# Performance work log

Hardware: AMD Instinct MI355X
Metric: run time of the kernel (lower is better)

## Reference

```python
import jax, jax.numpy as jnp
import numpy as np

B, T, H, HW = 16, 32, 512, 32  # batch, timesteps, hidden channels, spatial size


def setup_inputs() -> dict:
    key = jax.random.key(0)
    k1, k2, k3, k4, k5 = jax.random.split(key, 5)
    x = jax.random.normal(k1, (B, T, HW, HW), dtype=jnp.float32)
    # cell conv: 1x1, (1 + H) -> 4H, with bias (k=1 default, padding 'same')
    W_conv = jax.random.normal(k2, (4 * H, 1 + H, 1, 1), dtype=jnp.float32) * 0.02
    b_conv = jax.random.normal(k3, (4 * H,), dtype=jnp.float32) * 0.02
    # post conv: 3x3, H -> 1, padding 'same'
    W_post = jax.random.normal(k4, (1, H, 3, 3), dtype=jnp.float32) * 0.02
    b_post = jax.random.normal(k5, (1,), dtype=jnp.float32) * 0.02
    return {"x": x, "W_conv": W_conv, "b_conv": b_conv, "W_post": W_post, "b_post": b_post}


def _post_conv(h, W_post, b_post):
    # NCHW 3x3 'same' conv
    y = jax.lax.conv_general_dilated(
        h, W_post, window_strides=(1, 1), padding="SAME",
        dimension_numbers=("NCHW", "OIHW", "NCHW"))
    return y + b_post[None, :, None, None]


def reference(x, W_conv, b_conv, W_post, b_post):
    Wc = W_conv[:, :, 0, 0]  # [4H, 1+H] -- 1x1 conv is a channel GEMM

    def step(carry, xt):
        h, c = carry  # [B,H,32,32] each; xt [B,1,32,32]
        z = jnp.concatenate([xt, h], axis=1)  # [B,1+H,32,32]
        gates = jnp.einsum("bchw,oc->bohw", z, Wc) + b_conv[None, :, None, None]
        i, f, o, g = jnp.split(gates, 4, axis=1)
        # Faithful to source (non-standard gating):
        c = jax.nn.sigmoid(f) * c + jax.nn.sigmoid(i) + jnp.tanh(g)
        h = jax.nn.sigmoid(o) + jnp.tanh(c)
        y = _post_conv(h, W_post, b_post)  # [B,1,32,32]
        return (h, c), y

    h0 = jnp.zeros((x.shape[0], H, HW, HW), dtype=x.dtype)
    c0 = jnp.zeros_like(h0)
    xs = x[:, :, None, :, :].transpose(1, 0, 2, 3, 4)  # [T,B,1,32,32]
    _, ys = jax.lax.scan(step, (h0, c0), xs)  # ys [T,B,1,32,32]
    out = ys[:, :, 0].transpose(1, 0, 2, 3)  # [B,T,32,32] == cat along dim=1
    return out
```

## Files before the change

kernel.cpp:

```cpp
#include <hip/hip_runtime.h>
#include <cstdint>
#include <cstddef>

#define B_    16
#define T_    32
#define H_    512
#define P_    1024
#define NPOS  16384
#define NG    2048

typedef __attribute__((ext_vector_type(8))) short short8;
typedef __attribute__((ext_vector_type(4))) float f32x4;

__device__ __forceinline__ unsigned short f2bf(float f) {
  uint32_t u = __float_as_uint(f);
  u += 0x7fffu + ((u >> 16) & 1u);
  return (unsigned short)(u >> 16);
}
__device__ __forceinline__ float bflo(uint32_t u) { return __uint_as_float(u << 16); }
__device__ __forceinline__ float bfhi(uint32_t u) { return __uint_as_float(u & 0xffff0000u); }

__device__ __forceinline__ float sigf(float x) {
  return __builtin_amdgcn_rcpf(1.0f + __expf(-x));
}
__device__ __forceinline__ float tanhf_(float x) {
  return 1.0f - 2.0f * __builtin_amdgcn_rcpf(__expf(2.0f * x) + 1.0f);
}

__device__ __forceinline__ void gload_lds16(const void* g, void* l) {
  __builtin_amdgcn_global_load_lds(
      (const __attribute__((address_space(1))) void*)g,
      (__attribute__((address_space(3))) void*)l, 16, 0, 0);
}

__global__ void repack_w(const float* __restrict__ Wc, const float* __restrict__ bconv,
                         unsigned short* __restrict__ Wp, float* __restrict__ w0x,
                         float* __restrict__ bx) {
  int idx = blockIdx.x * 256 + threadIdx.x;
  int r = idx >> 9, k = idx & 511;
  int ch = r >> 2, g = r & 3;
  int o = g * 512 + ch;
  Wp[idx] = f2bf(Wc[o * 513 + 1 + k]);
  if (k == 0) { w0x[r] = Wc[o * 513]; bx[r] = bconv[o]; }
}

__global__ void repack_wpost(const float* __restrict__ Wpost, float* __restrict__ wpp) {
  int idx = blockIdx.x * 256 + threadIdx.x;
  if (idx >= 9 * 512) return;
  int j = idx >> 9, c = idx & 511;
  wpp[idx] = Wpost[c * 9 + j];
}

__global__ __launch_bounds__(256, 2)
void lstm_step(const unsigned short* __restrict__ Wp,
               const unsigned short* __restrict__ hprev,
               unsigned short* __restrict__ hnext,
               _Float16* __restrict__ Cst,
               const float* __restrict__ w0x, const float* __restrict__ bxv,
               const float* __restrict__ xin, int t) {
  __shared__ unsigned short As[256 * 64];
  __shared__ unsigned short Bs[128 * 64];

  const int tid = threadIdx.x;
  const int lane = tid & 63;
  const int wv = tid >> 6;
  const int wm = wv >> 1, wn = wv & 1;
  const int q = lane >> 4, l = lane & 15;

  const int r0 = blockIdx.x * 256;
  const int n0 = blockIdx.y * 128;

  const int srow = tid >> 3;
  const int lchunk = (tid & 7) ^ (srow & 7);
  const unsigned short* gA = Wp    + (size_t)(r0 + srow) * 512 + lchunk * 8;
  const unsigned short* gB = hprev + (size_t)(n0 + srow) * 512 + lchunk * 8;
  char* lA = (char*)As + wv * 1024;
  char* lB = (char*)Bs + wv * 1024;

  f32x4 acc[8][4] = {};

  for (int kc = 0; kc < 512; kc += 64) {
#pragma unroll
    for (int j = 0; j < 8; ++j)
      gload_lds16(gA + (size_t)j * (32 * 512) + kc, lA + j * 4096);
#pragma unroll
    for (int j = 0; j < 4; ++j)
      gload_lds16(gB + (size_t)j * (32 * 512) + kc, lB + j * 4096);
    __syncthreads();

#pragma unroll
    for (int kk = 0; kk < 2; ++kk) {
      short8 af[8], bf_[4];
#pragma unroll
      for (int mi = 0; mi < 8; ++mi) {
        int row = wm * 128 + mi * 16 + l;
        int sidx = row * 64 + (((kk * 4 + q) ^ (row & 7)) * 8);
        af[mi] = *(const short8*)(As + sidx);
      }
#pragma unroll
      for (int ni = 0; ni < 4; ++ni) {
        int row = wn * 64 + ni * 16 + l;
        int sidx = row * 64 + (((kk * 4 + q) ^ (row & 7)) * 8);
        bf_[ni] = *(const short8*)(Bs + sidx);
      }
#pragma unroll
      for (int mi = 0; mi < 8; ++mi)
#pragma unroll
        for (int ni = 0; ni < 4; ++ni)
          acc[mi][ni] = __builtin_amdgcn_mfma_f32_16x16x32_bf16(af[mi], bf_[ni], acc[mi][ni], 0, 0, 0);
    }
    __syncthreads();
  }

  float xv[4]; int posL[4]; size_t cbase[4];
#pragma unroll
  for (int ni = 0; ni < 4; ++ni) {
    posL[ni] = wn * 64 + ni * 16 + l;
    int pos = n0 + posL[ni];
    int b = pos >> 10, p = pos & 1023;
    xv[ni] = xin[((b * T_ + t) << 10) + p];
    cbase[ni] = ((size_t)b << 19) + p;
  }
  const int ch0 = blockIdx.x * 64;
#pragma unroll
  for (int mi = 0; mi < 8; ++mi) {
    int chl = wm * 32 + mi * 4 + q;
    int rg = r0 + wm * 128 + mi * 16 + q * 4;
    float4 w0 = *(const float4*)(w0x + rg);
    float4 bb = *(const float4*)(bxv + rg);
    int ch = ch0 + chl;
#pragma unroll
    for (int ni = 0; ni < 4; ++ni) {
      f32x4 g = acc[mi][ni];
      float gi = g[0] + w0.x * xv[ni] + bb.x;
      float gf = g[1] + w0.y * xv[ni] + bb.y;
      float go = g[2] + w0.z * xv[ni] + bb.z;
      float gg = g[3] + w0.w * xv[ni] + bb.w;
      size_t cidx = cbase[ni] + ((size_t)ch << 10);
      float cold = (float)Cst[cidx];
      float cn = sigf(gf) * cold + sigf(gi) + tanhf_(gg);
      float hn = sigf(go) + tanhf_(cn);
      Cst[cidx] = (_Float16)cn;
      As[posL[ni] * 64 + chl] = f2bf(hn);
    }
  }
  __syncthreads();
  {
    int pl = tid >> 1;
    int chh = (tid & 1) << 5;
    const uint4* src = (const uint4*)(As + pl * 64 + chh);
    unsigned short* dst = hnext + (size_t)(n0 + pl) * 512 + ch0 + chh;
    ((uint4*)dst)[0] = src[0];
    ((uint4*)dst)[1] = src[1];
    ((uint4*)dst)[2] = src[2];
    ((uint4*)dst)[3] = src[3];
  }
}

__global__ __launch_bounds__(256)
void post_conv(const unsigned short* __restrict__ h, const float* __restrict__ wpp,
               const float* __restrict__ bpost, float* __restrict__ out, int t) {
  int wid = blockIdx.x * 4 + (threadIdx.x >> 6);
  int lane = threadIdx.x & 63;
  int b = wid >> 10, p = wid & 1023;
  int py = p >> 5, px = p & 31;
  int c0 = lane << 3;
  float acc = 0.f;
#pragma unroll
  for (int dy = -1; dy <= 1; ++dy) {
    int ny = py + dy;
    if ((unsigned)ny > 31u) continue;
#pragma unroll
    for (int dx = -1; dx <= 1; ++dx) {
      int nx = px + dx;
      if ((unsigned)nx > 31u) continue;
      int j = (dy + 1) * 3 + (dx + 1);
      const uint4 hv = *(const uint4*)(h + ((size_t)((b << 10) + (ny << 5) + nx) << 9) + c0);
      const float4 wa = *(const float4*)(wpp + (j << 9) + c0);
      const float4 wb = *(const float4*)(wpp + (j << 9) + c0 + 4);
      acc += bflo(hv.x) * wa.x + bfhi(hv.x) * wa.y
           + bflo(hv.y) * wa.z + bfhi(hv.y) * wa.w
           + bflo(hv.z) * wb.x + bfhi(hv.z) * wb.y
           + bflo(hv.w) * wb.z + bfhi(hv.w) * wb.w;
    }
  }
#pragma unroll
  for (int off = 1; off < 64; off <<= 1)
    acc += __shfl_xor(acc, off, 64);
  if (lane == 0)
    out[((b * T_ + t) << 10) + p] = acc + bpost[0];
}

extern "C" void kernel_launch(void* const* d_in, const int* in_sizes, int n_in,
                              void* d_out, int out_size, void* d_ws, size_t ws_size,
                              hipStream_t stream) {
  const float* x     = (const float*)d_in[0];
  const float* Wconv = (const float*)d_in[1];
  const float* bconv = (const float*)d_in[2];
  const float* Wpost = (const float*)d_in[3];
  const float* bpost = (const float*)d_in[4];
  float* out = (float*)d_out;
  char* ws = (char*)d_ws;

  unsigned short* h0  = (unsigned short*)(ws);
  unsigned short* h1  = (unsigned short*)(ws + 16777216);
  _Float16*       Cst = (_Float16*)(ws + 33554432);
  unsigned short* Wp  = (unsigned short*)(ws + 50331648);
  float*          w0x = (float*)(ws + 52428800);
  float*          bx  = (float*)(ws + 52436992);
  float*          wpp = (float*)(ws + 52445184);

  hipMemsetAsync(h0, 0, 16777216, stream);
  hipMemsetAsync(Cst, 0, 16777216, stream);
  repack_w<<<4096, 256, 0, stream>>>(Wconv, bconv, Wp, w0x, bx);
  repack_wpost<<<18, 256, 0, stream>>>(Wpost, wpp);

  unsigned short* hp = h0;
  unsigned short* hn = h1;
  for (int t = 0; t < T_; ++t) {
    lstm_step<<<dim3(8, 128), 256, 0, stream>>>(Wp, hp, hn, Cst, w0x, bx, x, t);
    post_conv<<<4096, 256, 0, stream>>>(hn, wpp, bpost, out, t);
    unsigned short* tmp = hp; hp = hn; hn = tmp;
  }
}
```

Before: 2.001 ms.

## Fuse post-conv of previous step into LSTM step kernel as extra blocks

Extra grid rows (blockIdx.y >= 8) compute the 3x3 post conv on the previous timestep's hidden state, inside the same launch as the current step's gate GEMM. A single trailing post_conv launch handles the last step. This removes one kernel launch per timestep and lets the conv overlap with the GEMM. The change also swaps grid dimensions so the position tile is the fast index, pads the LDS staging stride from 64 to 72 to cut bank conflicts, and uses nontemporal loads and stores for the streaming x, cell state and output. The conv blocks now compete with the GEMM blocks for CUs, and the swapped block order changes L2 reuse of weights versus hidden state.

After: 2.067 ms. 3.3% more time.

```diff
diff --git a/kernel.cpp b/kernel.cpp
--- a/kernel.cpp
+++ b/kernel.cpp
@@ -57,18 +57,59 @@
                unsigned short* __restrict__ hnext,
                _Float16* __restrict__ Cst,
                const float* __restrict__ w0x, const float* __restrict__ bxv,
-               const float* __restrict__ xin, int t) {
+               const float* __restrict__ xin,
+               const float* __restrict__ wpp, const float* __restrict__ bpost,
+               float* __restrict__ out, int t) {
   __shared__ unsigned short As[256 * 64];
   __shared__ unsigned short Bs[128 * 64];
 
   const int tid = threadIdx.x;
   const int lane = tid & 63;
   const int wv = tid >> 6;
+
+  if (blockIdx.y >= 8) {
+    if (t == 0) return;
+    int quarter = blockIdx.y - 8;
+    int base = blockIdx.x * 128 + quarter * 32 + wv * 8;
+    int c0 = lane << 3;
+#pragma unroll
+    for (int e = 0; e < 8; ++e) {
+      int pos = base + e;
+      int b = pos >> 10, p = pos & 1023;
+      int py = p >> 5, px = p & 31;
+      float acc = 0.f;
+#pragma unroll
+      for (int dy = -1; dy <= 1; ++dy) {
+        int ny = py + dy;
+        if ((unsigned)ny > 31u) continue;
+#pragma unroll
+        for (int dx = -1; dx <= 1; ++dx) {
+          int nx = px + dx;
+          if ((unsigned)nx > 31u) continue;
+          int j = (dy + 1) * 3 + (dx + 1);
+          const uint4 hv = *(const uint4*)(hprev + ((size_t)((b << 10) + (ny << 5) + nx) << 9) + c0);
+          const float4 wa = *(const float4*)(wpp + (j << 9) + c0);
+          const float4 wb = *(const float4*)(wpp + (j << 9) + c0 + 4);
+          acc += bflo(hv.x) * wa.x + bfhi(hv.x) * wa.y
+               + bflo(hv.y) * wa.z + bfhi(hv.y) * wa.w
+               + bflo(hv.z) * wb.x + bfhi(hv.z) * wb.y
+               + bflo(hv.w) * wb.z + bfhi(hv.w) * wb.w;
+        }
+      }
+#pragma unroll
+      for (int off = 1; off < 64; off <<= 1)
+        acc += __shfl_xor(acc, off, 64);
+      if (lane == 0)
+        __builtin_nontemporal_store(acc + bpost[0], out + (((b * T_ + (t - 1)) << 10) + p));
+    }
+    return;
+  }
+
   const int wm = wv >> 1, wn = wv & 1;
   const int q = lane >> 4, l = lane & 15;
 
-  const int r0 = blockIdx.x * 256;
-  const int n0 = blockIdx.y * 128;
+  const int r0 = blockIdx.y * 256;
+  const int n0 = blockIdx.x * 128;
 
   const int srow = tid >> 3;
   const int lchunk = (tid & 7) ^ (srow & 7);
@@ -118,10 +159,10 @@
     posL[ni] = wn * 64 + ni * 16 + l;
     int pos = n0 + posL[ni];
     int b = pos >> 10, p = pos & 1023;
-    xv[ni] = xin[((b * T_ + t) << 10) + p];
+    xv[ni] = __builtin_nontemporal_load(xin + (((b * T_ + t) << 10) + p));
     cbase[ni] = ((size_t)b << 19) + p;
   }
-  const int ch0 = blockIdx.x * 64;
+  const int ch0 = blockIdx.y * 64;
 #pragma unroll
   for (int mi = 0; mi < 8; ++mi) {
     int chl = wm * 32 + mi * 4 + q;
@@ -137,18 +178,18 @@
       float go = g[2] + w0.z * xv[ni] + bb.z;
       float gg = g[3] + w0.w * xv[ni] + bb.w;
       size_t cidx = cbase[ni] + ((size_t)ch << 10);
-      float cold = (float)Cst[cidx];
+      float cold = (float)__builtin_nontemporal_load(Cst + cidx);
       float cn = sigf(gf) * cold + sigf(gi) + tanhf_(gg);
       float hn = sigf(go) + tanhf_(cn);
-      Cst[cidx] = (_Float16)cn;
-      As[posL[ni] * 64 + chl] = f2bf(hn);
+      __builtin_nontemporal_store((_Float16)cn, Cst + cidx);
+      As[posL[ni] * 72 + chl] = f2bf(hn);
     }
   }
   __syncthreads();
   {
     int pl = tid >> 1;
     int chh = (tid & 1) << 5;
-    const uint4* src = (const uint4*)(As + pl * 64 + chh);
+    const uint4* src = (const uint4*)(As + pl * 72 + chh);
     unsigned short* dst = hnext + (size_t)(n0 + pl) * 512 + ch0 + chh;
     ((uint4*)dst)[0] = src[0];
     ((uint4*)dst)[1] = src[1];
@@ -218,8 +259,9 @@
   unsigned short* hp = h0;
   unsigned short* hn = h1;
   for (int t = 0; t < T_; ++t) {
-    lstm_step<<<dim3(8, 128), 256, 0, stream>>>(Wp, hp, hn, Cst, w0x, bx, x, t);
-    post_conv<<<4096, 256, 0, stream>>>(hn, wpp, bpost, out, t);
+    lstm_step<<<dim3(128, 12), 256, 0, stream>>>(Wp, hp, hn, Cst, w0x, bx, x,
+                                                 wpp, bpost, out, t);
     unsigned short* tmp = hp; hp = hn; hn = tmp;
   }
-}
+  post_conv<<<4096, 256, 0, stream>>>(hp, wpp, bpost, out, T_ - 1);
+}
```

## Double-buffer LSTM GEMM K-tiles, lane-contiguous cell-state layout, padded h stash

Applied to the files above, without the earlier changes.

The GEMM main loop is restructured into a double-buffered pipeline with 32-wide K tiles. The next tile's global-to-LDS loads are issued right after the barrier, so they overlap the MFMA work on the current buffer, and one barrier per iteration is removed. The cell-state tensor gets a new layout indexed by lane so that its fp16 reads and writes are contiguous per wavefront. The h staging area is padded to a row stride of 72 to reduce LDS bank conflicts. LDS footprint stays the same, but the K loop now runs twice as many iterations with smaller tiles.

Result: slower. 2.301 ms (+15.0%).

```diff
diff --git a/kernel.cpp b/kernel.cpp
--- a/kernel.cpp
+++ b/kernel.cpp
@@ -58,8 +58,8 @@
                _Float16* __restrict__ Cst,
                const float* __restrict__ w0x, const float* __restrict__ bxv,
                const float* __restrict__ xin, int t) {
-  __shared__ unsigned short As[256 * 64];
-  __shared__ unsigned short Bs[128 * 64];
+  __shared__ unsigned short As[2][8192];
+  __shared__ unsigned short Bs[2][4096];
 
   const int tid = threadIdx.x;
   const int lane = tid & 63;
@@ -70,65 +70,69 @@
   const int r0 = blockIdx.x * 256;
   const int n0 = blockIdx.y * 128;
 
-  const int srow = tid >> 3;
-  const int lchunk = (tid & 7) ^ (srow & 7);
-  const unsigned short* gA = Wp    + (size_t)(r0 + srow) * 512 + lchunk * 8;
-  const unsigned short* gB = hprev + (size_t)(n0 + srow) * 512 + lchunk * 8;
-  char* lA = (char*)As + wv * 1024;
-  char* lB = (char*)Bs + wv * 1024;
+  const int srow = tid >> 2;
+  const int schunk = (tid & 3) ^ ((srow >> 1) & 3);
+  const unsigned short* gAt = Wp    + (size_t)(r0 + srow) * 512 + schunk * 8;
+  const unsigned short* gBt = hprev + (size_t)(n0 + srow) * 512 + schunk * 8;
 
   f32x4 acc[8][4] = {};
 
-  for (int kc = 0; kc < 512; kc += 64) {
-#pragma unroll
-    for (int j = 0; j < 8; ++j)
-      gload_lds16(gA + (size_t)j * (32 * 512) + kc, lA + j * 4096);
-#pragma unroll
-    for (int j = 0; j < 4; ++j)
-      gload_lds16(gB + (size_t)j * (32 * 512) + kc, lB + j * 4096);
+#define STAGE(buf, kc) do {                                                   \
+    _Pragma("unroll")                                                         \
+    for (int j = 0; j < 4; ++j)                                               \
+      gload_lds16(gAt + (size_t)j * 32768 + (kc),                             \
+                  (char*)As[buf] + j * 4096 + wv * 1024);                     \
+    _Pragma("unroll")                                                         \
+    for (int j = 0; j < 2; ++j)                                               \
+      gload_lds16(gBt + (size_t)j * 32768 + (kc),                             \
+                  (char*)Bs[buf] + j * 4096 + wv * 1024);                     \
+  } while (0)
+
+  STAGE(0, 0);
+  for (int it = 0; it < 16; ++it) {
     __syncthreads();
-
-#pragma unroll
-    for (int kk = 0; kk < 2; ++kk) {
-      short8 af[8], bf_[4];
-#pragma unroll
-      for (int mi = 0; mi < 8; ++mi) {
-        int row = wm * 128 + mi * 16 + l;
-        int sidx = row * 64 + (((kk * 4 + q) ^ (row & 7)) * 8);
-        af[mi] = *(const short8*)(As + sidx);
-      }
-#pragma unroll
-      for (int ni = 0; ni < 4; ++ni) {
-        int row = wn * 64 + ni * 16 + l;
-        int sidx = row * 64 + (((kk * 4 + q) ^ (row & 7)) * 8);
-        bf_[ni] = *(const short8*)(Bs + sidx);
-      }
-#pragma unroll
-      for (int mi = 0; mi < 8; ++mi)
-#pragma unroll
-        for (int ni = 0; ni < 4; ++ni)
-          acc[mi][ni] = __builtin_amdgcn_mfma_f32_16x16x32_bf16(af[mi], bf_[ni], acc[mi][ni], 0, 0, 0);
-    }
-    __syncthreads();
-  }
-
-  float xv[4]; int posL[4]; size_t cbase[4];
+    if (it < 15) STAGE((it + 1) & 1, (it + 1) * 32);
+
+    const unsigned short* Ab = As[it & 1];
+    const unsigned short* Bb = Bs[it & 1];
+    short8 af[8], bfr[4];
+#pragma unroll
+    for (int mi = 0; mi < 8; ++mi) {
+      int r = wm * 128 + mi * 16 + l;
+      af[mi] = *(const short8*)(Ab + r * 32 + ((q ^ ((r >> 1) & 3)) << 3));
+    }
+#pragma unroll
+    for (int ni = 0; ni < 4; ++ni) {
+      int r = wn * 64 + ni * 16 + l;
+      bfr[ni] = *(const short8*)(Bb + r * 32 + ((q ^ ((r >> 1) & 3)) << 3));
+    }
+#pragma unroll
+    for (int mi = 0; mi < 8; ++mi)
+#pragma unroll
+      for (int ni = 0; ni < 4; ++ni)
+        acc[mi][ni] = __builtin_amdgcn_mfma_f32_16x16x32_bf16(af[mi], bfr[ni], acc[mi][ni], 0, 0, 0);
+  }
+  __syncthreads();
+#undef STAGE
+
+  unsigned short* stash = (unsigned short*)As;
+  const int bI = n0 >> 10;
+  const int pg0 = (n0 & 1023) >> 4;
+  float xv[4]; int posL[4];
 #pragma unroll
   for (int ni = 0; ni < 4; ++ni) {
     posL[ni] = wn * 64 + ni * 16 + l;
-    int pos = n0 + posL[ni];
-    int b = pos >> 10, p = pos & 1023;
-    xv[ni] = xin[((b * T_ + t) << 10) + p];
-    cbase[ni] = ((size_t)b << 19) + p;
+    int p = (n0 & 1023) + posL[ni];
+    xv[ni] = xin[((bI * T_ + t) << 10) + p];
   }
   const int ch0 = blockIdx.x * 64;
+  const size_t cgb = ((size_t)bI * 128 + (ch0 >> 2) + wm * 8) * 64 + pg0 + wn * 4;
 #pragma unroll
   for (int mi = 0; mi < 8; ++mi) {
     int chl = wm * 32 + mi * 4 + q;
     int rg = r0 + wm * 128 + mi * 16 + q * 4;
     float4 w0 = *(const float4*)(w0x + rg);
     float4 bb = *(const float4*)(bxv + rg);
-    int ch = ch0 + chl;
 #pragma unroll
     for (int ni = 0; ni < 4; ++ni) {
       f32x4 g = acc[mi][ni];
@@ -136,19 +140,19 @@
       float gf = g[1] + w0.y * xv[ni] + bb.y;
       float go = g[2] + w0.z * xv[ni] + bb.z;
       float gg = g[3] + w0.w * xv[ni] + bb.w;
-      size_t cidx = cbase[ni] + ((size_t)ch << 10);
+      size_t cidx = ((cgb + (size_t)mi * 64 + ni) << 6) + lane;
       float cold = (float)Cst[cidx];
       float cn = sigf(gf) * cold + sigf(gi) + tanhf_(gg);
       float hn = sigf(go) + tanhf_(cn);
       Cst[cidx] = (_Float16)cn;
-      As[posL[ni] * 64 + chl] = f2bf(hn);
+      stash[posL[ni] * 72 + chl] = f2bf(hn);
     }
   }
   __syncthreads();
   {
     int pl = tid >> 1;
     int chh = (tid & 1) << 5;
-    const uint4* src = (const uint4*)(As + pl * 64 + chh);
+    const uint4* src = (const uint4*)(stash + pl * 72 + chh);
     unsigned short* dst = hnext + (size_t)(n0 + pl) * 512 + ch0 + chh;
     ((uint4*)dst)[0] = src[0];
     ((uint4*)dst)[1] = src[1];
```
